# Kernel optimization log

Measured on AMD Instinct MI355X. Metric: run time of the kernel, lower is better.

## Reference

```python
import math
import jax, jax.numpy as jnp
import numpy as np

N_HEAD = 16

def skew(QEr):
    # QEr: (B, H, L, L) where last dim indexes relative positions via Er_t
    B, H, L, _ = QEr.shape
    padded = jnp.pad(QEr, ((0, 0), (0, 0), (0, 0), (1, 0)))        # (B,H,L,L+1)
    reshaped = padded.reshape(B, H, L + 1, L)                       # (B,H,L+1,L)
    return reshaped[:, :, 1:, :]                                    # (B,H,L,L)

def setup_inputs() -> dict:
    key = jax.random.key(0)
    ks = jax.random.split(key, 6)
    B, L, D = 2, 2048, 1024
    hs = D // N_HEAD
    block_size = 2048
    return {
        "x": jax.random.normal(ks[0], (B, L, D), dtype=jnp.float32),
        "W_attn": jax.random.normal(ks[1], (D, 3 * D), dtype=jnp.float32) * 0.02,
        "b_attn": jnp.zeros((3 * D,), dtype=jnp.float32),
        "W_proj": jax.random.normal(ks[2], (D, D), dtype=jnp.float32) * 0.02,
        "b_proj": jnp.zeros((D,), dtype=jnp.float32),
        "Er": jax.random.normal(ks[3], (block_size, hs), dtype=jnp.float32),
    }

def reference(x, W_attn, b_attn, W_proj, b_proj, Er):
    B, L, D = x.shape
    H = N_HEAD
    hs = D // H
    qkv = x @ W_attn + b_attn                                       # (B,L,3D)
    q, k, v = jnp.split(qkv, 3, axis=-1)
    q = q.reshape(B, L, H, hs).transpose(0, 2, 1, 3)                # (B,H,L,hs)
    k = k.reshape(B, L, H, hs).transpose(0, 2, 1, 3)
    v = v.reshape(B, L, H, hs).transpose(0, 2, 1, 3)
    start = Er.shape[0] - L
    Er_t = Er[start:, :].T                                          # (hs,L)
    QEr = jnp.einsum('bhld,de->bhle', q, Er_t)                      # (B,H,L,L)
    Srel = skew(QEr)
    QK_t = jnp.einsum('bhqd,bhkd->bhqk', q, k)
    scale = 1.0 / math.sqrt(hs)
    att = (QK_t + Srel) * scale
    causal = jnp.tril(jnp.ones((L, L), dtype=bool))
    att = jnp.where(causal[None, None, :, :], att, -jnp.inf)
    att = jax.nn.softmax(att, axis=-1)
    y = jnp.einsum('bhqk,bhkd->bhqd', att, v)                       # (B,H,L,hs)
    y = y.transpose(0, 2, 1, 3).reshape(B, L, D)
    return y @ W_proj + b_proj
```

## Files before the change

kernel.cpp:

```cpp
#include <hip/hip_runtime.h>
#include <stdint.h>

#define L_SEQ 2048
#define D_MODEL 1024
#define NHEAD 16
#define HS 64
#define B_BATCH 2
#define QSCALE 0.1803368801111243f

typedef __bf16 bf16x8 __attribute__((ext_vector_type(8)));
typedef float f32x4 __attribute__((ext_vector_type(4)));

__device__ __forceinline__ float fexp2(float x) {
  return __builtin_amdgcn_exp2f(x);
}

__device__ __forceinline__ unsigned short f2b(float f) {
  unsigned int u = __float_as_uint(f);
  u += 0x7fffu + ((u >> 16) & 1u);
  return (unsigned short)(u >> 16);
}
__device__ __forceinline__ unsigned int pk2(float a, float b) {
  return (unsigned int)f2b(a) | ((unsigned int)f2b(b) << 16);
}

union U8 { uint4 v; unsigned short s[8]; };

__device__ __forceinline__ void ldsload16(const unsigned short* g, unsigned short* l) {
  __builtin_amdgcn_global_load_lds(
      (const __attribute__((address_space(1))) unsigned int*)g,
      (__attribute__((address_space(3))) unsigned int*)l, 16, 0, 0);
}

__device__ __forceinline__ bf16x8 frag_ld(const unsigned short* base, int row, int ks, int quad) {
  const int unit = (ks * 4 + quad) ^ (row & 7);
  return *(const bf16x8*)(base + row * 64 + unit * 8);
}

__global__ __launch_bounds__(256) void prep(
    const float* __restrict__ x, const float* __restrict__ Wa,
    const float* __restrict__ Wp, const float* __restrict__ Er,
    unsigned short* __restrict__ xb, unsigned short* __restrict__ wabT,
    unsigned short* __restrict__ wpbT, unsigned short* __restrict__ erb) {
  __shared__ unsigned short tt[64][65];
  int gb = blockIdx.x;
  if (gb < 2048) {
    int i = gb * 256 + threadIdx.x;
    const float4* s4 = (const float4*)x;
    float4 a = s4[i * 2], b = s4[i * 2 + 1];
    U8 u;
    u.s[0] = f2b(a.x); u.s[1] = f2b(a.y); u.s[2] = f2b(a.z); u.s[3] = f2b(a.w);
    u.s[4] = f2b(b.x); u.s[5] = f2b(b.y); u.s[6] = f2b(b.z); u.s[7] = f2b(b.w);
    ((uint4*)xb)[i] = u.v;
    return;
  }
  gb -= 2048;
  if (gb < 66) {
    int i = gb * 256 + threadIdx.x;
    if (i < 16384) {
      const float4* s4 = (const float4*)Er;
      float4 a = s4[i * 2], b = s4[i * 2 + 1];
      U8 u;
      u.s[0] = f2b(a.x); u.s[1] = f2b(a.y); u.s[2] = f2b(a.z); u.s[3] = f2b(a.w);
      u.s[4] = f2b(b.x); u.s[5] = f2b(b.y); u.s[6] = f2b(b.z); u.s[7] = f2b(b.w);
      ((uint4*)erb)[i] = u.v;
    } else {
      ((uint4*)erb)[i] = make_uint4(0u, 0u, 0u, 0u);
    }
    return;
  }
  gb -= 66;
  const float* src;
  unsigned short* dst;
  int N, nbx;
  if (gb < 768) { src = Wa; dst = wabT; N = 3072; nbx = 48; }
  else { gb -= 768; src = Wp; dst = wpbT; N = 1024; nbx = 16; }
  const int n0 = (gb % nbx) * 64, k0 = (gb / nbx) * 64;
  const int c = threadIdx.x & 63, r0 = threadIdx.x >> 6;
#pragma unroll
  for (int i = 0; i < 16; i++) {
    int r = r0 * 16 + i;
    tt[r][c] = f2b(src[(size_t)(k0 + r) * N + n0 + c]);
  }
  __syncthreads();
  const int n = threadIdx.x >> 2, ks = (threadIdx.x & 3) * 16;
  U8 u0, u1;
#pragma unroll
  for (int j = 0; j < 8; j++) {
    u0.s[j] = tt[ks + j][n];
    u1.s[j] = tt[ks + 8 + j][n];
  }
  unsigned short* d = dst + (size_t)(n0 + n) * 1024 + k0 + ks;
  *(uint4*)d = u0.v;
  *(uint4*)(d + 8) = u1.v;
}

__global__ __launch_bounds__(256, 3) void gemm_qkv(
    const unsigned short* __restrict__ A, const unsigned short* __restrict__ Bt,
    const float* __restrict__ bias, unsigned short* __restrict__ qbuf,
    unsigned short* __restrict__ kbuf, unsigned short* __restrict__ vbufT,
    int M, int N, int K) {
  __shared__ unsigned short As[128 * 64];
  __shared__ unsigned short Bs[128 * 64];
  const int tid = threadIdx.x, lane = tid & 63, w = tid >> 6;
  const int wm = w >> 1, wn = w & 1, quad = lane >> 4, lc = lane & 15;
  const int bm = blockIdx.y, bn = blockIdx.x;
  const int l8 = lane >> 3, u8 = ((lane & 7) ^ l8) * 8;
  const unsigned short* Ab = A + (size_t)bm * 128 * K;
  const unsigned short* Bb = Bt + (size_t)bn * 128 * K;

  f32x4 z4 = {0.f, 0.f, 0.f, 0.f};
  f32x4 acc[4][4];
#pragma unroll
  for (int mb = 0; mb < 4; mb++)
#pragma unroll
    for (int nb = 0; nb < 4; nb++) acc[mb][nb] = z4;

  for (int kk = 0; kk < K; kk += 64) {
    if (kk) __syncthreads();
#pragma unroll
    for (int i = 0; i < 4; i++) {
      int ch = w * 4 + i;
      ldsload16(Ab + (size_t)(ch * 8 + l8) * K + kk + u8, &As[ch * 512]);
      ldsload16(Bb + (size_t)(ch * 8 + l8) * K + kk + u8, &Bs[ch * 512]);
    }
    __syncthreads();
#pragma unroll
    for (int ks = 0; ks < 2; ks++) {
      bf16x8 af[4], bfv[4];
#pragma unroll
      for (int mb = 0; mb < 4; mb++) af[mb] = frag_ld(As, wm * 64 + mb * 16 + lc, ks, quad);
#pragma unroll
      for (int nb = 0; nb < 4; nb++) bfv[nb] = frag_ld(Bs, wn * 64 + nb * 16 + lc, ks, quad);
#pragma unroll
      for (int mb = 0; mb < 4; mb++)
#pragma unroll
        for (int nb = 0; nb < 4; nb++)
          acc[mb][nb] = __builtin_amdgcn_mfma_f32_16x16x32_bf16(af[mb], bfv[nb],
                                                               acc[mb][nb], 0, 0, 0);
    }
  }

#pragma unroll
  for (int nb = 0; nb < 4; nb++) {
    const int n = bn * 128 + wn * 64 + nb * 16 + lc;
    const float bv = bias[n];
    const int which = n >> 10;
    const int rem = n & 1023;
    const int h = rem >> 6, d = rem & 63;
    const float sc = which == 0 ? QSCALE : 1.0f;
#pragma unroll
    for (int mb = 0; mb < 4; mb++) {
#pragma unroll
      for (int reg = 0; reg < 4; reg++) {
        const int m = bm * 128 + wm * 64 + mb * 16 + quad * 4 + reg;
        const int b = m >> 11, l = m & 2047;
        float val = (acc[mb][nb][reg] + bv) * sc;
        if (which == 0)
          qbuf[((size_t)(b * NHEAD + h) * L_SEQ + l) * HS + d] = f2b(val);
        else if (which == 1)
          kbuf[((size_t)(b * NHEAD + h) * L_SEQ + l) * HS + d] = f2b(val);
        else
          vbufT[((size_t)(b * NHEAD + h) * HS + d) * L_SEQ + l] = f2b(val);
      }
    }
  }
}

__global__ __launch_bounds__(256, 2) void gemm_proj(
    const unsigned short* __restrict__ A, const unsigned short* __restrict__ Bt,
    const float* __restrict__ bias, float* __restrict__ out, int M, int N, int K) {
  __shared__ unsigned short As[128 * 64];
  __shared__ unsigned short Bs[64 * 64];
  const int tid = threadIdx.x, lane = tid & 63, w = tid >> 6;
  const int quad = lane >> 4, lc = lane & 15;
  const int bm = blockIdx.y, bn = blockIdx.x;
  const int l8 = lane >> 3, u8 = ((lane & 7) ^ l8) * 8;
  const unsigned short* Ab = A + (size_t)bm * 128 * K;
  const unsigned short* Bb = Bt + (size_t)bn * 64 * K;

  f32x4 z4 = {0.f, 0.f, 0.f, 0.f};
  f32x4 acc[2][4];
#pragma unroll
  for (int mb = 0; mb < 2; mb++)
#pragma unroll
    for (int nb = 0; nb < 4; nb++) acc[mb][nb] = z4;

  for (int kk = 0; kk < K; kk += 64) {
    if (kk) __syncthreads();
#pragma unroll
    for (int i = 0; i < 4; i++) {
      int ch = w * 4 + i;
      ldsload16(Ab + (size_t)(ch * 8 + l8) * K + kk + u8, &As[ch * 512]);
    }
#pragma unroll
    for (int i = 0; i < 2; i++) {
      int ch = w * 2 + i;
      ldsload16(Bb + (size_t)(ch * 8 + l8) * K + kk + u8, &Bs[ch * 512]);
    }
    __syncthreads();
#pragma unroll
    for (int ks = 0; ks < 2; ks++) {
      bf16x8 af[2], bfv[4];
#pragma unroll
      for (int mb = 0; mb < 2; mb++) af[mb] = frag_ld(As, w * 32 + mb * 16 + lc, ks, quad);
#pragma unroll
      for (int nb = 0; nb < 4; nb++) bfv[nb] = frag_ld(Bs, nb * 16 + lc, ks, quad);
#pragma unroll
      for (int mb = 0; mb < 2; mb++)
#pragma unroll
        for (int nb = 0; nb < 4; nb++)
          acc[mb][nb] = __builtin_amdgcn_mfma_f32_16x16x32_bf16(af[mb], bfv[nb],
                                                               acc[mb][nb], 0, 0, 0);
    }
  }

#pragma unroll
  for (int nb = 0; nb < 4; nb++) {
    const int n = bn * 64 + nb * 16 + lc;
    const float bv = bias[n];
#pragma unroll
    for (int mb = 0; mb < 2; mb++) {
#pragma unroll
      for (int reg = 0; reg < 4; reg++) {
        const int m = bm * 128 + w * 32 + mb * 16 + quad * 4 + reg;
        out[(size_t)m * N + n] = acc[mb][nb][reg] + bv;
      }
    }
  }
}

__global__ __launch_bounds__(256, 3) void flash_attn_rel(
    const unsigned short* __restrict__ qb, const unsigned short* __restrict__ kb,
    const unsigned short* __restrict__ vbT, const unsigned short* __restrict__ erb,
    unsigned short* __restrict__ yb) {
  __shared__ unsigned short Ks[64 * 64];
  __shared__ unsigned short Vt[64 * 64];
  __shared__ unsigned short Es[128 * 64];
  __shared__ float Twf[4][16 * 84];

  const int tid = threadIdx.x, lane = tid & 63, w = tid >> 6;
  const int quad = lane >> 4, lc = lane & 15;
  const int bh = blockIdx.x;
  const int b = bh >> 4, h = bh & 15;
  const int qt = 31 - (int)blockIdx.y;
  const int q0 = qt * 64;
  const int qg0 = q0 + w * 16;
  const size_t hoff = (size_t)bh * L_SEQ * HS;
  float* TwfW = Twf[w];
  unsigned short* TwpW = (unsigned short*)TwfW;
  const int l8 = lane >> 3, u8 = ((lane & 7) ^ l8) * 8;
  const f32x4 z4 = {0.f, 0.f, 0.f, 0.f};

  bf16x8 qf[2];
  {
    const unsigned short* qrow = qb + hoff + (size_t)(qg0 + lc) * HS;
    qf[0] = *(const bf16x8*)(qrow + quad * 8);
    qf[1] = *(const bf16x8*)(qrow + 32 + quad * 8);
  }
  f32x4 Oacc[4];
#pragma unroll
  for (int db = 0; db < 4; db++) Oacc[db] = z4;
  float psum_acc = 0.0f;

  const unsigned short* kgb = kb + hoff;
  const unsigned short* vgbT = vbT + (size_t)bh * HS * L_SEQ;
  const int ebw = 48 - w * 16;

  for (int k0 = 0; k0 <= q0; k0 += 64) {
    __syncthreads();
#pragma unroll
    for (int i = 0; i < 2; i++) {
      int ch = w * 2 + i;
      ldsload16(kgb + (size_t)(k0 + ch * 8 + l8) * HS + u8, &Ks[ch * 512]);
      ldsload16(vgbT + (size_t)(ch * 8 + l8) * L_SEQ + k0 + u8, &Vt[ch * 512]);
    }
    const int e0 = (L_SEQ - 64) - q0 + k0;
#pragma unroll
    for (int i = 0; i < 4; i++) {
      int ch = w * 4 + i;
      ldsload16(erb + (size_t)(e0 + ch * 8 + l8) * HS + u8, &Es[ch * 512]);
    }
    __syncthreads();

    f32x4 sacc[4], tacc[5];
#pragma unroll
    for (int i = 0; i < 4; i++) sacc[i] = z4;
#pragma unroll
    for (int i = 0; i < 5; i++) tacc[i] = z4;
#pragma unroll
    for (int ks = 0; ks < 2; ks++) {
#pragma unroll
      for (int kbi = 0; kbi < 4; kbi++) {
        bf16x8 a = frag_ld(Ks, kbi * 16 + lc, ks, quad);
        sacc[kbi] = __builtin_amdgcn_mfma_f32_16x16x32_bf16(a, qf[ks], sacc[kbi], 0, 0, 0);
      }
#pragma unroll
      for (int eb = 0; eb < 5; eb++) {
        bf16x8 a = frag_ld(Es, ebw + eb * 16 + lc, ks, quad);
        tacc[eb] = __builtin_amdgcn_mfma_f32_16x16x32_bf16(a, qf[ks], tacc[eb], 0, 0, 0);
      }
    }
#pragma unroll
    for (int eb = 0; eb < 5; eb++)
      *(f32x4*)&TwfW[lc * 84 + eb * 16 + quad * 4] = tacc[eb];
    asm volatile("" ::: "memory");

    float p[4][4], ps = 0.0f;
    const int tbase = lc * 84 + (15 - lc);
    if (k0 == q0) {
      const int qrow = w * 16 + lc;
#pragma unroll
      for (int kbi = 0; kbi < 4; kbi++)
#pragma unroll
        for (int reg = 0; reg < 4; reg++) {
          const int kk = kbi * 16 + quad * 4 + reg;
          float t = TwfW[tbase + kk];
          float v = (kk > qrow) ? -1e30f : (sacc[kbi][reg] + t);
          p[kbi][reg] = fexp2(v);
          ps += p[kbi][reg];
        }
    } else {
#pragma unroll
      for (int kbi = 0; kbi < 4; kbi++)
#pragma unroll
        for (int reg = 0; reg < 4; reg++) {
          float t = TwfW[tbase + kbi * 16 + quad * 4 + reg];
          p[kbi][reg] = fexp2(sacc[kbi][reg] + t);
          ps += p[kbi][reg];
        }
    }
    psum_acc += ps;
#pragma unroll
    for (int kbi = 0; kbi < 4; kbi++) {
      uint2 pk;
      pk.x = pk2(p[kbi][0], p[kbi][1]);
      pk.y = pk2(p[kbi][2], p[kbi][3]);
      const int k = kbi * 16 + quad * 4;
      *(uint2*)&TwpW[lc * 64 + (((k >> 3) ^ (lc & 7)) << 3) + (k & 7)] = pk;
    }
    asm volatile("" ::: "memory");

#pragma unroll
    for (int ks = 0; ks < 2; ks++) {
      bf16x8 pf = frag_ld(TwpW, lc, ks, quad);
#pragma unroll
      for (int db = 0; db < 4; db++) {
        bf16x8 av = frag_ld(Vt, db * 16 + lc, ks, quad);
        Oacc[db] = __builtin_amdgcn_mfma_f32_16x16x32_bf16(av, pf, Oacc[db], 0, 0, 0);
      }
    }
  }

  psum_acc += __shfl_xor(psum_acc, 16, 64);
  psum_acc += __shfl_xor(psum_acc, 32, 64);
  const float inv = 1.0f / psum_acc;

  __syncthreads();
  unsigned short* Yt = Es;
#pragma unroll
  for (int db = 0; db < 4; db++) {
    uint2 pk;
    pk.x = pk2(Oacc[db][0] * inv, Oacc[db][1] * inv);
    pk.y = pk2(Oacc[db][2] * inv, Oacc[db][3] * inv);
    *(uint2*)&Yt[(w * 16 + lc) * 72 + db * 16 + quad * 4] = pk;
  }
  __syncthreads();
  {
    const int r = tid >> 2, seg = (tid & 3) * 16;
    uint4 a0 = *(const uint4*)&Yt[r * 72 + seg];
    uint4 a1 = *(const uint4*)&Yt[r * 72 + seg + 8];
    unsigned short* d = yb + (size_t)((size_t)b * L_SEQ + q0 + r) * D_MODEL + h * HS + seg;
    *(uint4*)d = a0;
    *(uint4*)(d + 8) = a1;
  }
}

extern "C" void kernel_launch(void* const* d_in, const int* in_sizes, int n_in,
                              void* d_out, int out_size, void* d_ws, size_t ws_size,
                              hipStream_t stream) {
  const float* x = (const float*)d_in[0];
  const float* W_attn = (const float*)d_in[1];
  const float* b_attn = (const float*)d_in[2];
  const float* W_proj = (const float*)d_in[3];
  const float* b_proj = (const float*)d_in[4];
  const float* Er = (const float*)d_in[5];
  float* out = (float*)d_out;

  const int n_x = B_BATCH * L_SEQ * D_MODEL;
  const int n_wa = D_MODEL * 3 * D_MODEL;
  const int n_wp = D_MODEL * D_MODEL;
  const int n_er_pad = (L_SEQ + 64) * HS;
  const int n_head = B_BATCH * NHEAD * L_SEQ * HS;

  unsigned short* xb = (unsigned short*)d_ws;
  unsigned short* wabT = xb + n_x;
  unsigned short* wpbT = wabT + n_wa;
  unsigned short* erb = wpbT + n_wp;
  unsigned short* qbuf = erb + n_er_pad;
  unsigned short* kbuf = qbuf + n_head;
  unsigned short* vbufT = kbuf + n_head;
  unsigned short* ybuf = vbufT + n_head;

  prep<<<3138, 256, 0, stream>>>(x, W_attn, W_proj, Er, xb, wabT, wpbT, erb);

  gemm_qkv<<<dim3(24, 32), 256, 0, stream>>>(xb, wabT, b_attn, qbuf, kbuf, vbufT,
                                             B_BATCH * L_SEQ, 3 * D_MODEL, D_MODEL);

  flash_attn_rel<<<dim3(B_BATCH * NHEAD, 32), 256, 0, stream>>>(qbuf, kbuf, vbufT,
                                                                erb, ybuf);

  gemm_proj<<<dim3(16, 32), 256, 0, stream>>>(ybuf, wpbT, b_proj, out,
                                              B_BATCH * L_SEQ, D_MODEL, D_MODEL);
}
```

Baseline: 197.3 us.

## Double-buffer attention tiles, pair causal query tiles, stage V transpose through LDS

Each attention block now processes two query tiles (j and 31-j), so per-block causal work is balanced, and the grid shrinks to 16 rows. K, V and Er tiles are double-buffered, so the next tile's global-to-LDS loads are issued before the current tile is computed, which hides load latency. The relative-position scratch moves from fp32 to bf16 in LDS to cut shared-memory use. Separately, the QKV GEMM writes the transposed V through swizzled LDS so the global stores are coalesced 16-byte writes instead of scattered 2-byte ones. In exchange, LDS per block roughly doubles and occupancy drops from 3 to 2 blocks, and rounding the Er term to bf16 adds precision loss.

```diff
diff --git a/kernel.cpp b/kernel.cpp
--- a/kernel.cpp
+++ b/kernel.cpp
@@ -20,6 +20,9 @@
   u += 0x7fffu + ((u >> 16) & 1u);
   return (unsigned short)(u >> 16);
 }
+__device__ __forceinline__ float b2f(unsigned short s) {
+  return __uint_as_float(((unsigned int)s) << 16);
+}
 __device__ __forceinline__ unsigned int pk2(float a, float b) {
   return (unsigned int)f2b(a) | ((unsigned int)f2b(b) << 16);
 }
@@ -35,6 +38,10 @@
 __device__ __forceinline__ bf16x8 frag_ld(const unsigned short* base, int row, int ks, int quad) {
   const int unit = (ks * 4 + quad) ^ (row & 7);
   return *(const bf16x8*)(base + row * 64 + unit * 8);
+}
+__device__ __forceinline__ bf16x8 frag_ld88(const unsigned short* base, int row, int ks, int quad) {
+  const int unit = (ks * 4 + quad) ^ (row & 7);
+  return *(const bf16x8*)(base + row * 88 + unit * 8);
 }
 
 __global__ __launch_bounds__(256) void prep(
@@ -100,8 +107,9 @@
     const float* __restrict__ bias, unsigned short* __restrict__ qbuf,
     unsigned short* __restrict__ kbuf, unsigned short* __restrict__ vbufT,
     int M, int N, int K) {
-  __shared__ unsigned short As[128 * 64];
-  __shared__ unsigned short Bs[128 * 64];
+  __shared__ unsigned short SMEM[2 * 128 * 64];
+  unsigned short* As = SMEM;
+  unsigned short* Bs = SMEM + 128 * 64;
   const int tid = threadIdx.x, lane = tid & 63, w = tid >> 6;
   const int wm = w >> 1, wn = w & 1, quad = lane >> 4, lc = lane & 15;
   const int bm = blockIdx.y, bn = blockIdx.x;
@@ -141,28 +149,57 @@
     }
   }
 
-#pragma unroll
-  for (int nb = 0; nb < 4; nb++) {
-    const int n = bn * 128 + wn * 64 + nb * 16 + lc;
-    const float bv = bias[n];
-    const int which = n >> 10;
-    const int rem = n & 1023;
+  if (bn < 16) {
+#pragma unroll
+    for (int nb = 0; nb < 4; nb++) {
+      const int n = bn * 128 + wn * 64 + nb * 16 + lc;
+      const float bv = bias[n];
+      const int which = n >> 10;
+      const int rem = n & 1023;
+      const int h = rem >> 6, d = rem & 63;
+      unsigned short* dst = which == 0 ? qbuf : kbuf;
+      const float sc = which == 0 ? QSCALE : 1.0f;
+#pragma unroll
+      for (int mb = 0; mb < 4; mb++) {
+#pragma unroll
+        for (int reg = 0; reg < 4; reg++) {
+          const int m = bm * 128 + wm * 64 + mb * 16 + quad * 4 + reg;
+          const int b = m >> 11, l = m & 2047;
+          float val = (acc[mb][nb][reg] + bv) * sc;
+          dst[((size_t)(b * NHEAD + h) * L_SEQ + l) * HS + d] = f2b(val);
+        }
+      }
+    }
+  } else {
+    __syncthreads();
+    unsigned short* Vs = SMEM;
+#pragma unroll
+    for (int nb = 0; nb < 4; nb++) {
+      const int n_loc = wn * 64 + nb * 16 + lc;
+      const float bv = bias[bn * 128 + n_loc];
+#pragma unroll
+      for (int mb = 0; mb < 4; mb++) {
+#pragma unroll
+        for (int reg = 0; reg < 4; reg++) {
+          const int m_loc = wm * 64 + mb * 16 + quad * 4 + reg;
+          Vs[n_loc * 128 + (((m_loc >> 3) ^ (n_loc & 15)) << 3) + (m_loc & 7)] =
+              f2b(acc[mb][nb][reg] + bv);
+        }
+      }
+    }
+    __syncthreads();
+    const int n_loc = tid >> 1, mh = tid & 1;
+    const int n_glob = bn * 128 + n_loc;
+    const int rem = n_glob & 1023;
     const int h = rem >> 6, d = rem & 63;
-    const float sc = which == 0 ? QSCALE : 1.0f;
-#pragma unroll
-    for (int mb = 0; mb < 4; mb++) {
-#pragma unroll
-      for (int reg = 0; reg < 4; reg++) {
-        const int m = bm * 128 + wm * 64 + mb * 16 + quad * 4 + reg;
-        const int b = m >> 11, l = m & 2047;
-        float val = (acc[mb][nb][reg] + bv) * sc;
-        if (which == 0)
-          qbuf[((size_t)(b * NHEAD + h) * L_SEQ + l) * HS + d] = f2b(val);
-        else if (which == 1)
-          kbuf[((size_t)(b * NHEAD + h) * L_SEQ + l) * HS + d] = f2b(val);
-        else
-          vbufT[((size_t)(b * NHEAD + h) * HS + d) * L_SEQ + l] = f2b(val);
-      }
+    const int b = bm >> 4;
+    unsigned short* dstb =
+        vbufT + ((size_t)(b * NHEAD + h) * HS + d) * L_SEQ + (bm & 15) * 128;
+#pragma unroll
+    for (int c = 0; c < 8; c++) {
+      const int cg = mh * 8 + c;
+      const int u = cg ^ (n_loc & 15);
+      *(uint4*)(dstb + cg * 8) = *(const uint4*)&Vs[n_loc * 128 + u * 8];
     }
   }
 }
@@ -230,149 +267,168 @@
   }
 }
 
-__global__ __launch_bounds__(256, 3) void flash_attn_rel(
+__global__ __launch_bounds__(256, 2) void flash_attn_rel(
     const unsigned short* __restrict__ qb, const unsigned short* __restrict__ kb,
     const unsigned short* __restrict__ vbT, const unsigned short* __restrict__ erb,
     unsigned short* __restrict__ yb) {
-  __shared__ unsigned short Ks[64 * 64];
-  __shared__ unsigned short Vt[64 * 64];
-  __shared__ unsigned short Es[128 * 64];
-  __shared__ float Twf[4][16 * 84];
+  __shared__ unsigned short Ks[2][64 * 64];
+  __shared__ unsigned short Vt[2][64 * 64];
+  __shared__ unsigned short Es[2][128 * 64];
+  __shared__ unsigned short TP[4 * 16 * 88];
 
   const int tid = threadIdx.x, lane = tid & 63, w = tid >> 6;
   const int quad = lane >> 4, lc = lane & 15;
   const int bh = blockIdx.x;
   const int b = bh >> 4, h = bh & 15;
-  const int qt = 31 - (int)blockIdx.y;
-  const int q0 = qt * 64;
-  const int qg0 = q0 + w * 16;
+  const int j = blockIdx.y;
+  const int qts0 = 31 - j, qts1 = j;
   const size_t hoff = (size_t)bh * L_SEQ * HS;
-  float* TwfW = Twf[w];
-  unsigned short* TwpW = (unsigned short*)TwfW;
+  unsigned short* TPw = TP + w * (16 * 88);
   const int l8 = lane >> 3, u8 = ((lane & 7) ^ l8) * 8;
   const f32x4 z4 = {0.f, 0.f, 0.f, 0.f};
-
-  bf16x8 qf[2];
-  {
-    const unsigned short* qrow = qb + hoff + (size_t)(qg0 + lc) * HS;
-    qf[0] = *(const bf16x8*)(qrow + quad * 8);
-    qf[1] = *(const bf16x8*)(qrow + 32 + quad * 8);
-  }
-  f32x4 Oacc[4];
-#pragma unroll
-  for (int db = 0; db < 4; db++) Oacc[db] = z4;
-  float psum_acc = 0.0f;
-
   const unsigned short* kgb = kb + hoff;
-  const unsigned short* vgbT = vbT + (size_t)bh * HS * L_SEQ;
+  const unsigned short* vgbT = vbT + hoff;
   const int ebw = 48 - w * 16;
 
-  for (int k0 = 0; k0 <= q0; k0 += 64) {
-    __syncthreads();
+  auto stage = [&](int q0s, int k0s, int bufi) {
 #pragma unroll
     for (int i = 0; i < 2; i++) {
       int ch = w * 2 + i;
-      ldsload16(kgb + (size_t)(k0 + ch * 8 + l8) * HS + u8, &Ks[ch * 512]);
-      ldsload16(vgbT + (size_t)(ch * 8 + l8) * L_SEQ + k0 + u8, &Vt[ch * 512]);
-    }
-    const int e0 = (L_SEQ - 64) - q0 + k0;
+      ldsload16(kgb + (size_t)(k0s + ch * 8 + l8) * HS + u8, &Ks[bufi][ch * 512]);
+      ldsload16(vgbT + (size_t)(ch * 8 + l8) * L_SEQ + k0s + u8, &Vt[bufi][ch * 512]);
+    }
+    const int e0 = (L_SEQ - 64) - q0s + k0s;
 #pragma unroll
     for (int i = 0; i < 4; i++) {
       int ch = w * 4 + i;
-      ldsload16(erb + (size_t)(e0 + ch * 8 + l8) * HS + u8, &Es[ch * 512]);
-    }
-    __syncthreads();
-
-    f32x4 sacc[4], tacc[5];
-#pragma unroll
-    for (int i = 0; i < 4; i++) sacc[i] = z4;
-#pragma unroll
-    for (int i = 0; i < 5; i++) tacc[i] = z4;
-#pragma unroll
-    for (int ks = 0; ks < 2; ks++) {
+      ldsload16(erb + (size_t)(e0 + ch * 8 + l8) * HS + u8, &Es[bufi][ch * 512]);
+    }
+  };
+
+  int buf = 0;
+  stage(qts0 * 64, 0, 0);
+
+#pragma unroll 1
+  for (int phase = 0; phase < 2; phase++) {
+    const int q0 = (phase == 0 ? qts0 : qts1) * 64;
+    const int qg0 = q0 + w * 16;
+
+    bf16x8 qf[2];
+    {
+      const unsigned short* qrow = qb + hoff + (size_t)(qg0 + lc) * HS;
+      qf[0] = *(const bf16x8*)(qrow + quad * 8);
+      qf[1] = *(const bf16x8*)(qrow + 32 + quad * 8);
+    }
+    f32x4 Oacc[4];
+#pragma unroll
+    for (int db = 0; db < 4; db++) Oacc[db] = z4;
+    float psum_acc = 0.0f;
+
+#pragma unroll 1
+    for (int k0 = 0; k0 <= q0; k0 += 64) {
+      __syncthreads();
+      if (k0 + 64 <= q0) stage(q0, k0 + 64, buf ^ 1);
+      else if (phase == 0) stage(qts1 * 64, 0, buf ^ 1);
+
+      const unsigned short* KsB = Ks[buf];
+      const unsigned short* VtB = Vt[buf];
+      const unsigned short* EsB = Es[buf];
+
+      f32x4 sacc[4], tacc[5];
+#pragma unroll
+      for (int i = 0; i < 4; i++) sacc[i] = z4;
+#pragma unroll
+      for (int i = 0; i < 5; i++) tacc[i] = z4;
+#pragma unroll
+      for (int ks = 0; ks < 2; ks++) {
+#pragma unroll
+        for (int kbi = 0; kbi < 4; kbi++) {
+          bf16x8 a = frag_ld(KsB, kbi * 16 + lc, ks, quad);
+          sacc[kbi] = __builtin_amdgcn_mfma_f32_16x16x32_bf16(a, qf[ks], sacc[kbi], 0, 0, 0);
+        }
+#pragma unroll
+        for (int eb = 0; eb < 5; eb++) {
+          bf16x8 a = frag_ld(EsB, ebw + eb * 16 + lc, ks, quad);
+          tacc[eb] = __builtin_amdgcn_mfma_f32_16x16x32_bf16(a, qf[ks], tacc[eb], 0, 0, 0);
+        }
+      }
+#pragma unroll
+      for (int eb = 0; eb < 5; eb++) {
+        uint2 pk;
+        pk.x = pk2(tacc[eb][0], tacc[eb][1]);
+        pk.y = pk2(tacc[eb][2], tacc[eb][3]);
+        *(uint2*)&TPw[lc * 88 + eb * 16 + quad * 4] = pk;
+      }
+      asm volatile("" ::: "memory");
+
+      float p[4][4], ps = 0.0f;
+      const int tbase = lc * 88 + (15 - lc);
+      if (k0 == q0) {
+        const int qrow = w * 16 + lc;
+#pragma unroll
+        for (int kbi = 0; kbi < 4; kbi++)
+#pragma unroll
+          for (int reg = 0; reg < 4; reg++) {
+            const int kk = kbi * 16 + quad * 4 + reg;
+            float t = b2f(TPw[tbase + kk]);
+            float v = (kk > qrow) ? -1e30f : (sacc[kbi][reg] + t);
+            p[kbi][reg] = fexp2(v);
+            ps += p[kbi][reg];
+          }
+      } else {
+#pragma unroll
+        for (int kbi = 0; kbi < 4; kbi++)
+#pragma unroll
+          for (int reg = 0; reg < 4; reg++) {
+            float t = b2f(TPw[tbase + kbi * 16 + quad * 4 + reg]);
+            p[kbi][reg] = fexp2(sacc[kbi][reg] + t);
+            ps += p[kbi][reg];
+          }
+      }
+      psum_acc += ps;
 #pragma unroll
       for (int kbi = 0; kbi < 4; kbi++) {
-        bf16x8 a = frag_ld(Ks, kbi * 16 + lc, ks, quad);
-        sacc[kbi] = __builtin_amdgcn_mfma_f32_16x16x32_bf16(a, qf[ks], sacc[kbi], 0, 0, 0);
-      }
-#pragma unroll
-      for (int eb = 0; eb < 5; eb++) {
-        bf16x8 a = frag_ld(Es, ebw + eb * 16 + lc, ks, quad);
-        tacc[eb] = __builtin_amdgcn_mfma_f32_16x16x32_bf16(a, qf[ks], tacc[eb], 0, 0, 0);
-      }
-    }
-#pragma unroll
-    for (int eb = 0; eb < 5; eb++)
-      *(f32x4*)&TwfW[lc * 84 + eb * 16 + quad * 4] = tacc[eb];
-    asm volatile("" ::: "memory");
-
-    float p[4][4], ps = 0.0f;
-    const int tbase = lc * 84 + (15 - lc);
-    if (k0 == q0) {
-      const int qrow = w * 16 + lc;
-#pragma unroll
-      for (int kbi = 0; kbi < 4; kbi++)
-#pragma unroll
-        for (int reg = 0; reg < 4; reg++) {
-          const int kk = kbi * 16 + quad * 4 + reg;
-          float t = TwfW[tbase + kk];
-          float v = (kk > qrow) ? -1e30f : (sacc[kbi][reg] + t);
-          p[kbi][reg] = fexp2(v);
-          ps += p[kbi][reg];
+        uint2 pk;
+        pk.x = pk2(p[kbi][0], p[kbi][1]);
+        pk.y = pk2(p[kbi][2], p[kbi][3]);
+        const int kk2 = kbi * 16 + quad * 4;
+        *(uint2*)&TPw[lc * 88 + (((kk2 >> 3) ^ (lc & 7)) << 3) + (kk2 & 7)] = pk;
+      }
+      asm volatile("" ::: "memory");
+
+#pragma unroll
+      for (int ks = 0; ks < 2; ks++) {
+        bf16x8 pf = frag_ld88(TPw, lc, ks, quad);
+#pragma unroll
+        for (int db = 0; db < 4; db++) {
+          bf16x8 av = frag_ld(VtB, db * 16 + lc, ks, quad);
+          Oacc[db] = __builtin_amdgcn_mfma_f32_16x16x32_bf16(av, pf, Oacc[db], 0, 0, 0);
         }
-    } else {
-#pragma unroll
-      for (int kbi = 0; kbi < 4; kbi++)
-#pragma unroll
-        for (int reg = 0; reg < 4; reg++) {
-          float t = TwfW[tbase + kbi * 16 + quad * 4 + reg];
-          p[kbi][reg] = fexp2(sacc[kbi][reg] + t);
-          ps += p[kbi][reg];
-        }
-    }
-    psum_acc += ps;
-#pragma unroll
-    for (int kbi = 0; kbi < 4; kbi++) {
+      }
+      buf ^= 1;
+    }
+
+    psum_acc += __shfl_xor(psum_acc, 16, 64);
+    psum_acc += __shfl_xor(psum_acc, 32, 64);
+    const float inv = 1.0f / psum_acc;
+    __syncthreads();
+    unsigned short* Yt = TP;
+#pragma unroll
+    for (int db = 0; db < 4; db++) {
       uint2 pk;
-      pk.x = pk2(p[kbi][0], p[kbi][1]);
-      pk.y = pk2(p[kbi][2], p[kbi][3]);
-      const int k = kbi * 16 + quad * 4;
-      *(uint2*)&TwpW[lc * 64 + (((k >> 3) ^ (lc & 7)) << 3) + (k & 7)] = pk;
-    }
-    asm volatile("" ::: "memory");
-
-#pragma unroll
-    for (int ks = 0; ks < 2; ks++) {
-      bf16x8 pf = frag_ld(TwpW, lc, ks, quad);
-#pragma unroll
-      for (int db = 0; db < 4; db++) {
-        bf16x8 av = frag_ld(Vt, db * 16 + lc, ks, quad);
-        Oacc[db] = __builtin_amdgcn_mfma_f32_16x16x32_bf16(av, pf, Oacc[db], 0, 0, 0);
-      }
-    }
-  }
-
-  psum_acc += __shfl_xor(psum_acc, 16, 64);
-  psum_acc += __shfl_xor(psum_acc, 32, 64);
-  const float inv = 1.0f / psum_acc;
-
-  __syncthreads();
-  unsigned short* Yt = Es;
-#pragma unroll
-  for (int db = 0; db < 4; db++) {
-    uint2 pk;
-    pk.x = pk2(Oacc[db][0] * inv, Oacc[db][1] * inv);
-    pk.y = pk2(Oacc[db][2] * inv, Oacc[db][3] * inv);
-    *(uint2*)&Yt[(w * 16 + lc) * 72 + db * 16 + quad * 4] = pk;
-  }
-  __syncthreads();
-  {
-    const int r = tid >> 2, seg = (tid & 3) * 16;
-    uint4 a0 = *(const uint4*)&Yt[r * 72 + seg];
-    uint4 a1 = *(const uint4*)&Yt[r * 72 + seg + 8];
-    unsigned short* d = yb + (size_t)((size_t)b * L_SEQ + q0 + r) * D_MODEL + h * HS + seg;
-    *(uint4*)d = a0;
-    *(uint4*)(d + 8) = a1;
+      pk.x = pk2(Oacc[db][0] * inv, Oacc[db][1] * inv);
+      pk.y = pk2(Oacc[db][2] * inv, Oacc[db][3] * inv);
+      *(uint2*)&Yt[(w * 16 + lc) * 72 + db * 16 + quad * 4] = pk;
+    }
+    __syncthreads();
+    {
+      const int r = tid >> 2, seg = (tid & 3) * 16;
+      uint4 a0 = *(const uint4*)&Yt[r * 72 + seg];
+      uint4 a1 = *(const uint4*)&Yt[r * 72 + seg + 8];
+      unsigned short* d = yb + (size_t)((size_t)b * L_SEQ + q0 + r) * D_MODEL + h * HS + seg;
+      *(uint4*)d = a0;
+      *(uint4*)(d + 8) = a1;
+    }
   }
 }
 
@@ -407,7 +463,7 @@
   gemm_qkv<<<dim3(24, 32), 256, 0, stream>>>(xb, wabT, b_attn, qbuf, kbuf, vbufT,
                                              B_BATCH * L_SEQ, 3 * D_MODEL, D_MODEL);
 
-  flash_attn_rel<<<dim3(B_BATCH * NHEAD, 32), 256, 0, stream>>>(qbuf, kbuf, vbufT,
+  flash_attn_rel<<<dim3(B_BATCH * NHEAD, 16), 256, 0, stream>>>(qbuf, kbuf, vbufT,
                                                                 erb, ybuf);
 
   gemm_proj<<<dim3(16, 32), 256, 0, stream>>>(ybuf, wpbT, b_proj, out,
```

Result: slower. 228.8 us (+16.0%).
